# Optimization experiments

Measured on AMD Instinct MI355X. Metric: run time of the kernel, lower is better.

Reference implementation:

```python
import jax, jax.numpy as jnp
import numpy as np

EPS = 1e-5

def _layernorm(x, w, b):
    mu = jnp.mean(x, axis=-1, keepdims=True)
    var = jnp.mean(jnp.square(x - mu), axis=-1, keepdims=True)
    return (x - mu) * jax.lax.rsqrt(var + EPS) * w + b

def setup_inputs() -> dict:
    key = jax.random.key(0)
    ks = jax.random.split(key, 8)
    B, N, D = 1, 512, 128
    x = jax.random.normal(ks[0], (B, N, N, D), dtype=jnp.float32)
    mask = jnp.ones((B, N, N), dtype=jnp.float32)
    # learned params (torch nn.Linear stores weight as (out, in))
    p_in_w = jax.random.normal(ks[1], (2 * D, D), dtype=jnp.float32) * (1.0 / np.sqrt(D))
    g_in_w = jax.random.normal(ks[2], (2 * D, D), dtype=jnp.float32) * 0.02
    p_out_w = jax.random.normal(ks[3], (D, D), dtype=jnp.float32) * 0.02
    g_out_w = jax.random.normal(ks[4], (D, D), dtype=jnp.float32) * 0.02
    norm_in_w = jnp.ones((D,), dtype=jnp.float32)
    norm_in_b = jnp.zeros((D,), dtype=jnp.float32)
    norm_out_w = jnp.ones((D,), dtype=jnp.float32)
    norm_out_b = jnp.zeros((D,), dtype=jnp.float32)
    return {"x": x, "mask": mask, "norm_in_w": norm_in_w, "norm_in_b": norm_in_b,
            "p_in_w": p_in_w, "g_in_w": g_in_w, "norm_out_w": norm_out_w,
            "norm_out_b": norm_out_b, "p_out_w": p_out_w, "g_out_w": g_out_w}

def reference(x, mask, norm_in_w, norm_in_b, p_in_w, g_in_w, norm_out_w, norm_out_b, p_out_w, g_out_w):
    # x: (B,N,N,D), mask: (B,N,N)
    x_ln = _layernorm(x, norm_in_w, norm_in_b)          # (B,N,N,D)
    x_in = x_ln
    # gated dual projection to 2D channels, then mask
    h = jnp.einsum('bijd,ed->bije', x_ln, p_in_w) * jax.nn.sigmoid(
        jnp.einsum('bijd,ed->bije', x_ln, g_in_w))      # (B,N,N,2D)
    h = h * mask[..., None]
    D = x.shape[-1]
    a, b = h[..., :D], h[..., D:]                        # (B,N,N,D) each
    # triangular 'outgoing' contraction over k
    t = jnp.einsum('bikd,bjkd->bijd', a, b)              # (B,N,N,D)
    out = jnp.einsum('bijd,ed->bije', _layernorm(t, norm_out_w, norm_out_b), p_out_w) \
        * jax.nn.sigmoid(jnp.einsum('bijd,ed->bije', x_in, g_out_w))
    return out
```

## Files before the change

kernel.cpp:

```cpp
#include <hip/hip_runtime.h>
#include <stdint.h>

#define NSEQ 512
#define DDIM 128
#define NROWS (NSEQ * NSEQ)
#define PMASK (NROWS - 1)
#define ROT(idx, d) (((idx) + (d) * 128) & PMASK)

typedef __bf16 bf16x8 __attribute__((ext_vector_type(8)));
typedef __bf16 bf16x2v __attribute__((ext_vector_type(2)));
typedef unsigned short u16;
typedef u16 ushort8 __attribute__((ext_vector_type(8)));
typedef float f32x4 __attribute__((ext_vector_type(4)));
typedef uint32_t u32x4 __attribute__((ext_vector_type(4)));
typedef uint32_t u32x2 __attribute__((ext_vector_type(2)));

__device__ __forceinline__ u16 cvt1(float f) {
  return __builtin_bit_cast(u16, (__bf16)f);
}
__device__ __forceinline__ uint32_t pk2(float a, float b) {
  bf16x2v v = {(__bf16)a, (__bf16)b};
  return __builtin_bit_cast(uint32_t, v);
}
__device__ __forceinline__ float bf2f(u16 u) {
  uint32_t x = ((uint32_t)u) << 16;
  return __builtin_bit_cast(float, x);
}
__device__ __forceinline__ f32x4 mfma_bf16(ushort8 a, ushort8 b, f32x4 c) {
  return __builtin_amdgcn_mfma_f32_16x16x32_bf16(
      __builtin_bit_cast(bf16x8, a), __builtin_bit_cast(bf16x8, b), c, 0, 0, 0);
}
__device__ __forceinline__ float sigmoidf_(float x) {
  return __builtin_amdgcn_rcpf(1.0f + __expf(-x));
}

#define ROR16(v, n)                                                            \
  __builtin_bit_cast(float, __builtin_amdgcn_update_dpp(                       \
      __builtin_bit_cast(int, (v)), __builtin_bit_cast(int, (v)),              \
      0x120 + (n), 0xF, 0xF, false))

#define GLOAD16(gp, lp)                                                        \
  __builtin_amdgcn_global_load_lds(                                            \
      (const __attribute__((address_space(1))) void*)(gp),                     \
      (__attribute__((address_space(3))) void*)(lp), 16, 0, 0)

__global__ __launch_bounds__(256) void k0_prep(
    const float* __restrict__ p_in_w, const float* __restrict__ g_in_w,
    const float* __restrict__ p_out_w, const float* __restrict__ g_out_w,
    const float* __restrict__ now, const float* __restrict__ nob,
    u16* __restrict__ Wb, u16* __restrict__ Pb, u16* __restrict__ Gb,
    float* __restrict__ S12) {
  const int b = blockIdx.x, t = threadIdx.x;
#pragma unroll
  for (int k = 0; k < 2; ++k) {
    const int idx = b * 512 + k * 256 + t;
    const float v = (idx < 32768) ? p_in_w[idx] : g_in_w[idx - 32768];
    Wb[idx] = cvt1(v);
  }
  if (t < 128) {
    const int idx = b * 128 + t;
    const int d = idx & 127;
    Pb[idx] = cvt1(p_out_w[idx] * now[d]);
    Gb[idx] = cvt1(g_out_w[idx]);
  }
  const int w = t >> 6, lane = t & 63;
  if (w >= 2) {
    const float* wv = (w == 2) ? now : nob;
    float p = p_out_w[b * 128 + lane] * wv[lane] +
              p_out_w[b * 128 + 64 + lane] * wv[64 + lane];
#pragma unroll
    for (int m = 1; m < 64; m <<= 1) p += __shfl_xor(p, m);
    if (lane == 0) S12[2 * b + (w - 2)] = p;
  }
}

__global__ __launch_bounds__(256, 6) void k1_ln_proj(
    const float* __restrict__ x, const float* __restrict__ mask,
    const float* __restrict__ niw, const float* __restrict__ nib,
    const u16* __restrict__ Wb, const u16* __restrict__ Gb,
    u16* __restrict__ AtB, u16* __restrict__ gArg) {
  __shared__ __align__(16) u16 xln[64 * 128];
  __shared__ __align__(16) u16 stage[64 * 64];
  const int tid = threadIdx.x;
  const int lane = tid & 63;
  const int w = tid >> 6;
  const int bid = blockIdx.x;
  const int rb = (bid >> 5) * 8 + (bid & 7);
  const int cg = (bid >> 3) & 3;
  const int r0 = rb * 64;
  const int g = lane >> 4, c = lane & 15;

  f32x4 v0[4], v1[4];
#pragma unroll
  for (int it = 0; it < 4; ++it) {
    const int rl = w * 16 + it * 4 + g;
    const float* xr = x + (size_t)(r0 + rl) * DDIM + c * 8;
    v0[it] = *(const f32x4*)xr;
    v1[it] = *(const f32x4*)(xr + 4);
  }
  const f32x4 w0 = *(const f32x4*)(niw + c * 8);
  const f32x4 w1 = *(const f32x4*)(niw + c * 8 + 4);
  const f32x4 b0 = *(const f32x4*)(nib + c * 8);
  const f32x4 b1 = *(const f32x4*)(nib + c * 8 + 4);
#pragma unroll
  for (int it = 0; it < 4; ++it) {
    const int rl = w * 16 + it * 4 + g;
    float s = v0[it][0] + v0[it][1] + v0[it][2] + v0[it][3] +
              v1[it][0] + v1[it][1] + v1[it][2] + v1[it][3];
    float ss = v0[it][0] * v0[it][0] + v0[it][1] * v0[it][1] +
               v0[it][2] * v0[it][2] + v0[it][3] * v0[it][3] +
               v1[it][0] * v1[it][0] + v1[it][1] * v1[it][1] +
               v1[it][2] * v1[it][2] + v1[it][3] * v1[it][3];
    { float t1 = ROR16(s, 1); s += t1; t1 = ROR16(ss, 1); ss += t1; }
    { float t1 = ROR16(s, 2); s += t1; t1 = ROR16(ss, 2); ss += t1; }
    { float t1 = ROR16(s, 4); s += t1; t1 = ROR16(ss, 4); ss += t1; }
    { float t1 = ROR16(s, 8); s += t1; t1 = ROR16(ss, 8); ss += t1; }
    const float mu = s * (1.0f / 128.0f);
    const float rs = rsqrtf(ss * (1.0f / 128.0f) - mu * mu + 1e-5f);
    float f0 = (v0[it][0] - mu) * rs * w0[0] + b0[0];
    float f1 = (v0[it][1] - mu) * rs * w0[1] + b0[1];
    float f2 = (v0[it][2] - mu) * rs * w0[2] + b0[2];
    float f3 = (v0[it][3] - mu) * rs * w0[3] + b0[3];
    float f4 = (v1[it][0] - mu) * rs * w1[0] + b1[0];
    float f5 = (v1[it][1] - mu) * rs * w1[1] + b1[1];
    float f6 = (v1[it][2] - mu) * rs * w1[2] + b1[2];
    float f7 = (v1[it][3] - mu) * rs * w1[3] + b1[3];
    u32x4 ov{pk2(f0, f1), pk2(f2, f3), pk2(f4, f5), pk2(f6, f7)};
    const int byteoff = rl * 256 + ((c ^ (rl & 7)) << 4);
    *(u32x4*)((char*)xln + byteoff) = ov;
  }
  __syncthreads();

  const int lr = lane & 15, lq = lane >> 4;
  const int eP = cg * 64 + w * 16;
  f32x4 accP[4], accG[4];
#pragma unroll
  for (int m = 0; m < 4; ++m) {
    accP[m] = f32x4{0.f, 0.f, 0.f, 0.f};
    accG[m] = f32x4{0.f, 0.f, 0.f, 0.f};
  }

#pragma unroll
  for (int ks = 0; ks < 4; ++ks) {
    const int kblk = ks * 4 + lq;
    ushort8 af[4];
#pragma unroll
    for (int m = 0; m < 4; ++m) {
      const int row = m * 16 + lr;
      af[m] = *(const ushort8*)((const char*)xln + row * 256 +
                                ((kblk ^ (row & 7)) << 4));
    }
    const int e = eP + lr;
    const int dd = ks * 32 + lq * 8;
    const ushort8 bP = *(const ushort8*)(Wb + e * 128 + dd);
    const ushort8 bG = *(const ushort8*)(Wb + (256 + e) * 128 + dd);
#pragma unroll
    for (int m = 0; m < 4; ++m) {
      accP[m] = mfma_bf16(af[m], bP, accP[m]);
      accG[m] = mfma_bf16(af[m], bG, accG[m]);
    }
  }

  const int dloc = w * 16 + lr;
#pragma unroll
  for (int m = 0; m < 4; ++m) {
    const int rloc = m * 16 + lq * 4;
    const f32x4 mv = *(const f32x4*)(mask + r0 + rloc);
    const float o0 = accP[m][0] * sigmoidf_(accG[m][0]) * mv[0];
    const float o1 = accP[m][1] * sigmoidf_(accG[m][1]) * mv[1];
    const float o2 = accP[m][2] * sigmoidf_(accG[m][2]) * mv[2];
    const float o3 = accP[m][3] * sigmoidf_(accG[m][3]) * mv[3];
    u32x2 pk;
    pk[0] = pk2(o0, o1);
    pk[1] = pk2(o2, o3);
    const int gsw = (m * 4 + lq) ^ (dloc & 15);
    *(u32x2*)((char*)stage + dloc * 128 + (gsw << 3)) = pk;
  }
  __syncthreads();

  {
    const int i_ = rb >> 3, kt = rb & 7;
    u16* dst = AtB + (((size_t)kt * 512 + i_) * 256 + cg * 64) * 64;
#pragma unroll
    for (int q = 0; q < 2; ++q) {
      const int e = q * 32 + (tid >> 3);
      const int g0 = (tid & 7) * 2;
      const u32x2 lo =
          *(const u32x2*)((const char*)stage + e * 128 + ((g0 ^ (e & 15)) << 3));
      const u32x2 hi = *(const u32x2*)((const char*)stage + e * 128 +
                                       (((g0 + 1) ^ (e & 15)) << 3));
      u32x4 outv{lo[0], lo[1], hi[0], hi[1]};
      *(u32x4*)(dst + e * 64 + (tid & 7) * 8) = outv;
    }
  }

  if (cg < 2) {
    f32x4 accO[4];
#pragma unroll
    for (int m = 0; m < 4; ++m) accO[m] = f32x4{0.f, 0.f, 0.f, 0.f};
    const int eg = cg * 64 + w * 16 + lr;
#pragma unroll
    for (int ks = 0; ks < 4; ++ks) {
      const int kblk = ks * 4 + lq;
      const ushort8 bO = *(const ushort8*)(Gb + eg * 128 + ks * 32 + lq * 8);
#pragma unroll
      for (int m = 0; m < 4; ++m) {
        const int row = m * 16 + lr;
        const ushort8 af2 = *(const ushort8*)((const char*)xln + row * 256 +
                                              ((kblk ^ (row & 7)) << 4));
        accO[m] = mfma_bf16(af2, bO, accO[m]);
      }
    }
    __syncthreads();
    u16* stage2 = stage;
    const int e_loc = w * 16 + lr;
    const int gsl = e_loc >> 2;
    const int esub = (e_loc & 3) * 2;
#pragma unroll
    for (int m = 0; m < 4; ++m) {
#pragma unroll
      for (int reg = 0; reg < 4; ++reg) {
        const int rl2 = m * 16 + lq * 4 + reg;
        *(u16*)((char*)stage2 + rl2 * 128 + ((gsl ^ (rl2 & 7)) << 3) + esub) =
            cvt1(accO[m][reg]);
      }
    }
    __syncthreads();
#pragma unroll
    for (int p = 0; p < 2; ++p) {
      const int r = p * 32 + (tid >> 3);
      const int il8 = tid & 7;
      const char* base = (const char*)stage2 + r * 128;
      const u32x2 a = *(const u32x2*)(base + (((il8 * 2) ^ (r & 7)) << 3));
      const u32x2 b = *(const u32x2*)(base + (((il8 * 2 + 1) ^ (r & 7)) << 3));
      u32x4 ov{a[0], a[1], b[0], b[1]};
      *(u32x4*)(gArg + (size_t)(r0 + r) * DDIM + cg * 64 + il8 * 8) = ov;
    }
  }
}

__global__ __launch_bounds__(256) void k2_tri(const u16* __restrict__ AtB,
                                              u16* __restrict__ Ct) {
  __shared__ __align__(16) u16 lds[2 * 16384];
  const int tid = threadIdx.x;
  const int bid = blockIdx.x;
  const int lb = (bid & 7) * 256 + (bid >> 3);
  const int d = lb >> 4;
  const int tile = lb & 15;
  const int i0 = (tile >> 2) * 128, j0 = (tile & 3) * 128;
  const int lane = tid & 63, wid = tid >> 6;
  const int wr = wid >> 1, wc = wid & 1;
  const int lr = lane & 15, lq = lane >> 4;

  f32x4 acc[4][4];
#pragma unroll
  for (int m = 0; m < 4; ++m)
#pragma unroll
    for (int n = 0; n < 4; ++n) acc[m][n] = f32x4{0.f, 0.f, 0.f, 0.f};

  auto stage = [&](int kt, int buf) {
#pragma unroll
    for (int q = 0; q < 4; ++q) {
      const int idx = q * 256 + tid;
      const int r = idx >> 3, bk = idx & 7;
      const int sbk = bk ^ (r & 7);
      GLOAD16(AtB + (((size_t)kt * 512 + i0 + r) * 256 + d) * 64 + sbk * 8,
              &lds[buf * 16384 + idx * 8]);
      GLOAD16(AtB + (((size_t)kt * 512 + j0 + r) * 256 + 128 + d) * 64 + sbk * 8,
              &lds[buf * 16384 + 8192 + idx * 8]);
    }
  };

  stage(0, 0);
  __syncthreads();
  for (int kt = 0; kt < 8; ++kt) {
    const int buf = kt & 1;
    if (kt < 7) stage(kt + 1, buf ^ 1);
    const u16* A_l = &lds[buf * 16384];
    const u16* B_l = &lds[buf * 16384 + 8192];
#pragma unroll
    for (int ks = 0; ks < 2; ++ks) {
      const int kblk = ks * 4 + lq;
      ushort8 af[4], bfr[4];
#pragma unroll
      for (int m = 0; m < 4; ++m) {
        const int row = wr * 64 + m * 16 + lr;
        af[m] = *(const ushort8*)((const char*)A_l + row * 128 +
                                  ((kblk ^ (row & 7)) << 4));
      }
#pragma unroll
      for (int n = 0; n < 4; ++n) {
        const int col = wc * 64 + n * 16 + lr;
        bfr[n] = *(const ushort8*)((const char*)B_l + col * 128 +
                                   ((kblk ^ (col & 7)) << 4));
      }
#pragma unroll
      for (int m = 0; m < 4; ++m)
#pragma unroll
        for (int n = 0; n < 4; ++n)
          acc[m][n] = mfma_bf16(af[m], bfr[n], acc[m][n]);
    }
    __syncthreads();
  }

  u16* Cd = Ct + (size_t)d * NROWS;
#pragma unroll
  for (int m = 0; m < 4; ++m) {
    const int i = i0 + wr * 64 + m * 16 + lq * 4;
#pragma unroll
    for (int n = 0; n < 4; ++n) {
      const int j = j0 + wc * 64 + n * 16 + lr;
#pragma unroll
      for (int reg = 0; reg < 4; ++reg)
        Cd[ROT((i + reg) * NSEQ + j, d)] = cvt1(acc[m][n][reg]);
    }
  }
}

__global__ __launch_bounds__(256, 4) void k3_out(
    const u16* __restrict__ Ct, const u16* __restrict__ gArg,
    const u16* __restrict__ Pb, const float* __restrict__ S12,
    float* __restrict__ out) {
  __shared__ __align__(16) u16 ldsT[128 * 128];
  __shared__ float ps[4 * 128], pss[4 * 128];
  __shared__ float prm[128 * 2];
  __shared__ float s12l[128 * 2];
  const int tid = threadIdx.x, lane = tid & 63, w = tid >> 6;
  const int c0 = blockIdx.x * 128;

  {
    const int row2 = lane * 2;
    float s0 = 0.f, ss0 = 0.f, s1 = 0.f, ss1 = 0.f;
#pragma unroll
    for (int db = 0; db < 4; ++db) {
      uint32_t pe[4], po[4];
#pragma unroll
      for (int j = 0; j < 8; ++j) {
        const int d = w * 32 + db * 8 + j;
        const uint32_t v = *(const uint32_t*)(Ct + (size_t)d * NROWS +
                                              ROT(c0 + row2, d));
        const u16 ue = (u16)v, uo = (u16)(v >> 16);
        const float fe = bf2f(ue), fo = bf2f(uo);
        s0 += fe; ss0 += fe * fe;
        s1 += fo; ss1 += fo * fo;
        if (j & 1) {
          pe[j >> 1] |= ((uint32_t)ue) << 16;
          po[j >> 1] |= ((uint32_t)uo) << 16;
        } else {
          pe[j >> 1] = ue;
          po[j >> 1] = uo;
        }
      }
      const int gr = w * 4 + db;
      *(u32x4*)((char*)ldsT + row2 * 256 + ((gr ^ (row2 & 7)) << 4)) =
          u32x4{pe[0], pe[1], pe[2], pe[3]};
      *(u32x4*)((char*)ldsT + (row2 + 1) * 256 + ((gr ^ ((row2 + 1) & 7)) << 4)) =
          u32x4{po[0], po[1], po[2], po[3]};
    }
    ps[w * 128 + row2] = s0;
    pss[w * 128 + row2] = ss0;
    ps[w * 128 + row2 + 1] = s1;
    pss[w * 128 + row2 + 1] = ss1;
  }
  if (tid < 128) ((u32x2*)s12l)[tid] = ((const u32x2*)S12)[tid];
  __syncthreads();
  if (tid < 128) {
    const float s = ps[tid] + ps[128 + tid] + ps[256 + tid] + ps[384 + tid];
    const float ss = pss[tid] + pss[128 + tid] + pss[256 + tid] + pss[384 + tid];
    const float mu = s * (1.f / 128.f);
    const float rs = rsqrtf(ss * (1.f / 128.f) - mu * mu + 1e-5f);
    prm[2 * tid] = rs;
    prm[2 * tid + 1] = -rs * mu;
  }

  const int lr = lane & 15, lq = lane >> 4;
  const int rowbase = w * 32;
  f32x4 aP[2][8];
#pragma unroll
  for (int m = 0; m < 2; ++m)
#pragma unroll
    for (int n = 0; n < 8; ++n) aP[m][n] = f32x4{0.f, 0.f, 0.f, 0.f};
#pragma unroll
  for (int ks = 0; ks < 4; ++ks) {
    const int kblk = ks * 4 + lq;
    ushort8 at2[2];
#pragma unroll
    for (int m = 0; m < 2; ++m) {
      const int row = rowbase + m * 16 + lr;
      at2[m] = *(const ushort8*)((const char*)ldsT + row * 256 +
                                 ((kblk ^ (row & 7)) << 4));
    }
    ushort8 bp[8];
#pragma unroll
    for (int n = 0; n < 8; ++n) {
      const int e = n * 16 + lr;
      bp[n] = *(const ushort8*)(Pb + e * 128 + ks * 32 + lq * 8);
    }
#pragma unroll
    for (int m = 0; m < 2; ++m)
#pragma unroll
      for (int n = 0; n < 8; ++n) aP[m][n] = mfma_bf16(at2[m], bp[n], aP[m][n]);
  }
  __syncthreads();

#pragma unroll
  for (int m = 0; m < 2; ++m) {
    const int crow = rowbase + m * 16 + lq * 4;
#pragma unroll
    for (int n = 0; n < 8; ++n) {
      const int e = n * 16 + lr;
      const float s1 = s12l[2 * e], s2v = s12l[2 * e + 1];
#pragma unroll
      for (int reg = 0; reg < 4; ++reg) {
        const float rs = prm[2 * (crow + reg)];
        const float t1 = prm[2 * (crow + reg) + 1];
        const float op = rs * aP[m][n][reg] + t1 * s1 + s2v;
        const size_t r = (size_t)(c0 + crow + reg);
        const float gt = sigmoidf_(bf2f(gArg[r * DDIM + e]));
        out[r * DDIM + e] = op * gt;
      }
    }
  }
}

extern "C" void kernel_launch(void* const* d_in, const int* in_sizes, int n_in,
                              void* d_out, int out_size, void* d_ws,
                              size_t ws_size, hipStream_t stream) {
  const float* x = (const float*)d_in[0];
  const float* mask = (const float*)d_in[1];
  const float* niw = (const float*)d_in[2];
  const float* nib = (const float*)d_in[3];
  const float* p_in_w = (const float*)d_in[4];
  const float* g_in_w = (const float*)d_in[5];
  const float* now = (const float*)d_in[6];
  const float* nob = (const float*)d_in[7];
  const float* p_out_w = (const float*)d_in[8];
  const float* g_out_w = (const float*)d_in[9];
  float* out = (float*)d_out;
  char* ws = (char*)d_ws;

  u16* AtB = (u16*)(ws);
  u16* Ct = (u16*)(ws + 134217728);
  u16* gA = (u16*)(ws + 201326592);
  u16* Wb = (u16*)(ws + 268435456);
  u16* Pb = (u16*)(ws + 268566528);
  u16* Gb = (u16*)(ws + 268599296);
  float* S12 = (float*)(ws + 268632064);

  hipLaunchKernelGGL(k0_prep, dim3(128), dim3(256), 0, stream, p_in_w, g_in_w,
                     p_out_w, g_out_w, now, nob, Wb, Pb, Gb, S12);
  hipLaunchKernelGGL(k1_ln_proj, dim3(4 * NROWS / 64), dim3(256), 0, stream, x,
                     mask, niw, nib, Wb, Gb, AtB, gA);
  hipLaunchKernelGGL(k2_tri, dim3(128 * 16), dim3(256), 0, stream, AtB, Ct);
  hipLaunchKernelGGL(k3_out, dim3(NROWS / 128), dim3(256), 0, stream, Ct, gA,
                     Pb, S12, out);
}
```

Baseline: 321.7 us.

## Factor input layernorm into weights and precompute bf16 x with row stats

Adds a pass that converts x to bf16 once and stores per-row rstd and -rstd*mu. The layernorm affine is folded into the projection weights plus per-output correction constants. k1 then loads bf16 x straight into LDS with global_load_lds instead of re-reading fp32 x and normalizing it in each of its four column-group blocks, and applies the row stats in the epilogue. This trades the 4x redundant fp32 reads and normalize math for an extra kernel launch and an extra bf16 write/read of x, which is staged in the output buffer. Matmuls on unnormalized x in bf16 may also lose precision when row means are large.

Result: slower. 349.2 us (+8.5%).

```diff
diff --git a/kernel.cpp b/kernel.cpp
--- a/kernel.cpp
+++ b/kernel.cpp
@@ -48,39 +48,109 @@
     const float* __restrict__ p_in_w, const float* __restrict__ g_in_w,
     const float* __restrict__ p_out_w, const float* __restrict__ g_out_w,
     const float* __restrict__ now, const float* __restrict__ nob,
+    const float* __restrict__ niw, const float* __restrict__ nib,
     u16* __restrict__ Wb, u16* __restrict__ Pb, u16* __restrict__ Gb,
-    float* __restrict__ S12) {
+    float* __restrict__ S12, float* __restrict__ C) {
   const int b = blockIdx.x, t = threadIdx.x;
 #pragma unroll
   for (int k = 0; k < 2; ++k) {
     const int idx = b * 512 + k * 256 + t;
+    const int d = idx & 127;
     const float v = (idx < 32768) ? p_in_w[idx] : g_in_w[idx - 32768];
-    Wb[idx] = cvt1(v);
+    Wb[idx] = cvt1(v * niw[d]);
   }
   if (t < 128) {
     const int idx = b * 128 + t;
     const int d = idx & 127;
     Pb[idx] = cvt1(p_out_w[idx] * now[d]);
-    Gb[idx] = cvt1(g_out_w[idx]);
+    Gb[idx] = cvt1(g_out_w[idx] * niw[d]);
   }
   const int w = t >> 6, lane = t & 63;
-  if (w >= 2) {
-    const float* wv = (w == 2) ? now : nob;
-    float p = p_out_w[b * 128 + lane] * wv[lane] +
-              p_out_w[b * 128 + 64 + lane] * wv[64 + lane];
-#pragma unroll
-    for (int m = 1; m < 64; m <<= 1) p += __shfl_xor(p, m);
-    if (lane == 0) S12[2 * b + (w - 2)] = p;
+  {
+    const int e = b * 4 + w;
+    const float* src = (e < 256) ? (p_in_w + e * 128) : (g_in_w + (e - 256) * 128);
+    const float v0 = src[lane], v1 = src[lane + 64];
+    float c1 = niw[lane] * v0 + niw[lane + 64] * v1;
+    float c2 = nib[lane] * v0 + nib[lane + 64] * v1;
+#pragma unroll
+    for (int m = 1; m < 64; m <<= 1) {
+      c1 += __shfl_xor(c1, m);
+      c2 += __shfl_xor(c2, m);
+    }
+    if (lane == 0) {
+      C[e] = c1;
+      C[512 + e] = c2;
+    }
+  }
+  if (w == 0) {
+    const float v0 = g_out_w[b * 128 + lane], v1 = g_out_w[b * 128 + 64 + lane];
+    float c1 = niw[lane] * v0 + niw[lane + 64] * v1;
+    float c2 = nib[lane] * v0 + nib[lane + 64] * v1;
+#pragma unroll
+    for (int m = 1; m < 64; m <<= 1) {
+      c1 += __shfl_xor(c1, m);
+      c2 += __shfl_xor(c2, m);
+    }
+    if (lane == 0) {
+      C[1024 + b] = c1;
+      C[1152 + b] = c2;
+    }
+  }
+  if (w == 1) {
+    const float p0 = p_out_w[b * 128 + lane], p1 = p_out_w[b * 128 + 64 + lane];
+    float s1 = p0 * now[lane] + p1 * now[lane + 64];
+    float s2 = p0 * nob[lane] + p1 * nob[lane + 64];
+#pragma unroll
+    for (int m = 1; m < 64; m <<= 1) {
+      s1 += __shfl_xor(s1, m);
+      s2 += __shfl_xor(s2, m);
+    }
+    if (lane == 0) {
+      S12[2 * b] = s1;
+      S12[2 * b + 1] = s2;
+    }
+  }
+}
+
+__global__ __launch_bounds__(256) void k0b_stats(const float* __restrict__ x,
+                                                 u16* __restrict__ xbf,
+                                                 float* __restrict__ stats) {
+  const int tid = threadIdx.x, lane = tid & 63, w = tid >> 6;
+  const int g = lane >> 4, c = lane & 15;
+  const int r0 = blockIdx.x * 64;
+#pragma unroll
+  for (int it = 0; it < 4; ++it) {
+    const int rl = w * 16 + it * 4 + g;
+    const float* xr = x + (size_t)(r0 + rl) * DDIM + c * 8;
+    const f32x4 v0 = *(const f32x4*)xr;
+    const f32x4 v1 = *(const f32x4*)(xr + 4);
+    float s = v0[0] + v0[1] + v0[2] + v0[3] + v1[0] + v1[1] + v1[2] + v1[3];
+    float ss = v0[0] * v0[0] + v0[1] * v0[1] + v0[2] * v0[2] + v0[3] * v0[3] +
+               v1[0] * v1[0] + v1[1] * v1[1] + v1[2] * v1[2] + v1[3] * v1[3];
+    { float t1 = ROR16(s, 1); s += t1; t1 = ROR16(ss, 1); ss += t1; }
+    { float t1 = ROR16(s, 2); s += t1; t1 = ROR16(ss, 2); ss += t1; }
+    { float t1 = ROR16(s, 4); s += t1; t1 = ROR16(ss, 4); ss += t1; }
+    { float t1 = ROR16(s, 8); s += t1; t1 = ROR16(ss, 8); ss += t1; }
+    const float mu = s * (1.0f / 128.0f);
+    const float rs = rsqrtf(ss * (1.0f / 128.0f) - mu * mu + 1e-5f);
+    u32x4 ov{pk2(v0[0], v0[1]), pk2(v0[2], v0[3]), pk2(v1[0], v1[1]),
+             pk2(v1[2], v1[3])};
+    *(u32x4*)(xbf + (size_t)(r0 + rl) * DDIM + c * 8) = ov;
+    if (c == 0) {
+      stats[2 * (r0 + rl)] = rs;
+      stats[2 * (r0 + rl) + 1] = -rs * mu;
+    }
   }
 }
 
 __global__ __launch_bounds__(256, 6) void k1_ln_proj(
-    const float* __restrict__ x, const float* __restrict__ mask,
-    const float* __restrict__ niw, const float* __restrict__ nib,
+    const u16* __restrict__ xbf, const float* __restrict__ mask,
+    const float* __restrict__ stats, const float* __restrict__ C,
     const u16* __restrict__ Wb, const u16* __restrict__ Gb,
     u16* __restrict__ AtB, u16* __restrict__ gArg) {
   __shared__ __align__(16) u16 xln[64 * 128];
   __shared__ __align__(16) u16 stage[64 * 64];
+  __shared__ float st[128];
   const int tid = threadIdx.x;
   const int lane = tid & 63;
   const int w = tid >> 6;
@@ -88,58 +158,28 @@
   const int rb = (bid >> 5) * 8 + (bid & 7);
   const int cg = (bid >> 3) & 3;
   const int r0 = rb * 64;
-  const int g = lane >> 4, c = lane & 15;
-
-  f32x4 v0[4], v1[4];
-#pragma unroll
-  for (int it = 0; it < 4; ++it) {
-    const int rl = w * 16 + it * 4 + g;
-    const float* xr = x + (size_t)(r0 + rl) * DDIM + c * 8;
-    v0[it] = *(const f32x4*)xr;
-    v1[it] = *(const f32x4*)(xr + 4);
-  }
-  const f32x4 w0 = *(const f32x4*)(niw + c * 8);
-  const f32x4 w1 = *(const f32x4*)(niw + c * 8 + 4);
-  const f32x4 b0 = *(const f32x4*)(nib + c * 8);
-  const f32x4 b1 = *(const f32x4*)(nib + c * 8 + 4);
-#pragma unroll
-  for (int it = 0; it < 4; ++it) {
-    const int rl = w * 16 + it * 4 + g;
-    float s = v0[it][0] + v0[it][1] + v0[it][2] + v0[it][3] +
-              v1[it][0] + v1[it][1] + v1[it][2] + v1[it][3];
-    float ss = v0[it][0] * v0[it][0] + v0[it][1] * v0[it][1] +
-               v0[it][2] * v0[it][2] + v0[it][3] * v0[it][3] +
-               v1[it][0] * v1[it][0] + v1[it][1] * v1[it][1] +
-               v1[it][2] * v1[it][2] + v1[it][3] * v1[it][3];
-    { float t1 = ROR16(s, 1); s += t1; t1 = ROR16(ss, 1); ss += t1; }
-    { float t1 = ROR16(s, 2); s += t1; t1 = ROR16(ss, 2); ss += t1; }
-    { float t1 = ROR16(s, 4); s += t1; t1 = ROR16(ss, 4); ss += t1; }
-    { float t1 = ROR16(s, 8); s += t1; t1 = ROR16(ss, 8); ss += t1; }
-    const float mu = s * (1.0f / 128.0f);
-    const float rs = rsqrtf(ss * (1.0f / 128.0f) - mu * mu + 1e-5f);
-    float f0 = (v0[it][0] - mu) * rs * w0[0] + b0[0];
-    float f1 = (v0[it][1] - mu) * rs * w0[1] + b0[1];
-    float f2 = (v0[it][2] - mu) * rs * w0[2] + b0[2];
-    float f3 = (v0[it][3] - mu) * rs * w0[3] + b0[3];
-    float f4 = (v1[it][0] - mu) * rs * w1[0] + b1[0];
-    float f5 = (v1[it][1] - mu) * rs * w1[1] + b1[1];
-    float f6 = (v1[it][2] - mu) * rs * w1[2] + b1[2];
-    float f7 = (v1[it][3] - mu) * rs * w1[3] + b1[3];
-    u32x4 ov{pk2(f0, f1), pk2(f2, f3), pk2(f4, f5), pk2(f6, f7)};
-    const int byteoff = rl * 256 + ((c ^ (rl & 7)) << 4);
-    *(u32x4*)((char*)xln + byteoff) = ov;
-  }
+
+#pragma unroll
+  for (int q = 0; q < 4; ++q) {
+    const int idx = q * 256 + tid;
+    const int rl = idx >> 4, gg = idx & 15;
+    GLOAD16(xbf + (size_t)(r0 + rl) * DDIM + ((gg ^ (rl & 7)) * 8),
+            &xln[idx * 8]);
+  }
+  if (tid < 128) st[tid] = stats[r0 * 2 + tid];
   __syncthreads();
 
   const int lr = lane & 15, lq = lane >> 4;
   const int eP = cg * 64 + w * 16;
+  const int ecol = eP + lr;
+  const float C1p = C[ecol], C2p = C[512 + ecol];
+  const float C1q = C[256 + ecol], C2q = C[768 + ecol];
   f32x4 accP[4], accG[4];
 #pragma unroll
   for (int m = 0; m < 4; ++m) {
     accP[m] = f32x4{0.f, 0.f, 0.f, 0.f};
     accG[m] = f32x4{0.f, 0.f, 0.f, 0.f};
   }
-
 #pragma unroll
   for (int ks = 0; ks < 4; ++ks) {
     const int kblk = ks * 4 + lq;
@@ -150,10 +190,9 @@
       af[m] = *(const ushort8*)((const char*)xln + row * 256 +
                                 ((kblk ^ (row & 7)) << 4));
     }
-    const int e = eP + lr;
     const int dd = ks * 32 + lq * 8;
-    const ushort8 bP = *(const ushort8*)(Wb + e * 128 + dd);
-    const ushort8 bG = *(const ushort8*)(Wb + (256 + e) * 128 + dd);
+    const ushort8 bP = *(const ushort8*)(Wb + ecol * 128 + dd);
+    const ushort8 bG = *(const ushort8*)(Wb + (256 + ecol) * 128 + dd);
 #pragma unroll
     for (int m = 0; m < 4; ++m) {
       accP[m] = mfma_bf16(af[m], bP, accP[m]);
@@ -166,13 +205,17 @@
   for (int m = 0; m < 4; ++m) {
     const int rloc = m * 16 + lq * 4;
     const f32x4 mv = *(const f32x4*)(mask + r0 + rloc);
-    const float o0 = accP[m][0] * sigmoidf_(accG[m][0]) * mv[0];
-    const float o1 = accP[m][1] * sigmoidf_(accG[m][1]) * mv[1];
-    const float o2 = accP[m][2] * sigmoidf_(accG[m][2]) * mv[2];
-    const float o3 = accP[m][3] * sigmoidf_(accG[m][3]) * mv[3];
+    float o[4];
+#pragma unroll
+    for (int j = 0; j < 4; ++j) {
+      const float rs = st[2 * (rloc + j)], t1 = st[2 * (rloc + j) + 1];
+      const float hP = rs * accP[m][j] + t1 * C1p + C2p;
+      const float hG = rs * accG[m][j] + t1 * C1q + C2q;
+      o[j] = hP * sigmoidf_(hG) * mv[j];
+    }
     u32x2 pk;
-    pk[0] = pk2(o0, o1);
-    pk[1] = pk2(o2, o3);
+    pk[0] = pk2(o[0], o[1]);
+    pk[1] = pk2(o[2], o[3]);
     const int gsw = (m * 4 + lq) ^ (dloc & 15);
     *(u32x2*)((char*)stage + dloc * 128 + (gsw << 3)) = pk;
   }
@@ -213,6 +256,7 @@
     }
     __syncthreads();
     u16* stage2 = stage;
+    const float C1Gv = C[1024 + eg], C2Gv = C[1152 + eg];
     const int e_loc = w * 16 + lr;
     const int gsl = e_loc >> 2;
     const int esub = (e_loc & 3) * 2;
@@ -221,8 +265,10 @@
 #pragma unroll
       for (int reg = 0; reg < 4; ++reg) {
         const int rl2 = m * 16 + lq * 4 + reg;
+        const float rs = st[2 * rl2], t1 = st[2 * rl2 + 1];
+        const float val = rs * accO[m][reg] + t1 * C1Gv + C2Gv;
         *(u16*)((char*)stage2 + rl2 * 128 + ((gsl ^ (rl2 & 7)) << 3) + esub) =
-            cvt1(accO[m][reg]);
+            cvt1(val);
       }
     }
     __syncthreads();
@@ -447,10 +493,16 @@
   u16* Gb = (u16*)(ws + 268599296);
   float* S12 = (float*)(ws + 268632064);
 
+  u16* xbf = (u16*)d_out;
+  float* stats = (float*)((char*)d_out + 67108864);
+  float* C = (float*)((char*)d_out + 69206016);
+
   hipLaunchKernelGGL(k0_prep, dim3(128), dim3(256), 0, stream, p_in_w, g_in_w,
-                     p_out_w, g_out_w, now, nob, Wb, Pb, Gb, S12);
-  hipLaunchKernelGGL(k1_ln_proj, dim3(4 * NROWS / 64), dim3(256), 0, stream, x,
-                     mask, niw, nib, Wb, Gb, AtB, gA);
+                     p_out_w, g_out_w, now, nob, niw, nib, Wb, Pb, Gb, S12, C);
+  hipLaunchKernelGGL(k0b_stats, dim3(NROWS / 64), dim3(256), 0, stream, x, xbf,
+                     stats);
+  hipLaunchKernelGGL(k1_ln_proj, dim3(4 * NROWS / 64), dim3(256), 0, stream,
+                     xbf, mask, stats, C, Wb, Gb, AtB, gA);
   hipLaunchKernelGGL(k2_tri, dim3(128 * 16), dim3(256), 0, stream, AtB, Ct);
   hipLaunchKernelGGL(k3_out, dim3(NROWS / 128), dim3(256), 0, stream, Ct, gA,
                      Pb, S12, out);
```
